# Kernel tuning notes

Measured on AMD Instinct MI355X. Metric: run time of the kernel, lower is better.

Reference implementation:

```python
import jax, jax.numpy as jnp
import numpy as np

B, S, H = 32, 512, 768          # batch, encoder seq len, hidden size
W, G = 128, 4                   # max words per example, max tokens per word group
NH, HD, FF, NL, NLAB = 4, 192, 2048, 2, 6  # heads, head dim, ffn dim, layers, labels
EPS = 1e-5


def setup_inputs() -> dict:
    key = jax.random.key(0)
    ks = jax.random.split(key, 16)
    s = 0.02
    hidden = jax.random.normal(ks[0], (B, S, H), jnp.float32)
    word_token_idx = jax.random.randint(ks[1], (B, W, G), 0, S).astype(jnp.int32)
    glen = jax.random.randint(ks[2], (B, W), 1, G + 1)
    group_token_mask = jnp.arange(G)[None, None, :] < glen[:, :, None]  # [B,W,G] bool
    nwords = jax.random.randint(ks[3], (B,), W // 2, W + 1)
    word_valid = jnp.arange(W)[None, :] < nwords[:, None]               # [B,W] bool
    return {
        'hidden': hidden,
        'word_token_idx': word_token_idx,
        'group_token_mask': group_token_mask,
        'word_valid': word_valid,
        'qkv_w': jax.random.normal(ks[4], (NL, 3 * H, H), jnp.float32) * s,
        'qkv_b': jnp.zeros((NL, 3 * H), jnp.float32),
        'out_w': jax.random.normal(ks[5], (NL, H, H), jnp.float32) * s,
        'out_b': jnp.zeros((NL, H), jnp.float32),
        'ff1_w': jax.random.normal(ks[6], (NL, FF, H), jnp.float32) * s,
        'ff1_b': jnp.zeros((NL, FF), jnp.float32),
        'ff2_w': jax.random.normal(ks[7], (NL, H, FF), jnp.float32) * s,
        'ff2_b': jnp.zeros((NL, H), jnp.float32),
        'ln1_s': jnp.ones((NL, H), jnp.float32),
        'ln1_b': jnp.zeros((NL, H), jnp.float32),
        'ln2_s': jnp.ones((NL, H), jnp.float32),
        'ln2_b': jnp.zeros((NL, H), jnp.float32),
        'cls_w': jax.random.normal(ks[8], (NLAB, H), jnp.float32) * s,
        'cls_b': jnp.zeros((NLAB,), jnp.float32),
    }


def _ln(x, s, b):
    m = x.mean(-1, keepdims=True)
    v = ((x - m) ** 2).mean(-1, keepdims=True)
    return (x - m) * jax.lax.rsqrt(v + EPS) * s + b


def reference(hidden, word_token_idx, group_token_mask, word_valid,
              qkv_w, qkv_b, out_w, out_b, ff1_w, ff1_b, ff2_w, ff2_b,
              ln1_s, ln1_b, ln2_s, ln2_b, cls_w, cls_b):
    dt = hidden.dtype
    # ragged per-word gather + masked mean over each subword group: [B,W,G,H]
    gathered = jax.vmap(lambda h, i: h[i])(hidden, word_token_idx)
    gm = group_token_mask[..., None].astype(dt)
    wemb = (gathered * gm).sum(2) / jnp.maximum(gm.sum(2), 1.0)   # [B,W,H]
    # invalid (padded) words are zero, matching torch pad_sequence zero-padding
    wemb = wemb * word_valid[..., None].astype(dt)
    cls = hidden[:, 0, :]
    x = jnp.concatenate([cls[:, None, :], wemb], axis=1)          # [B, W+1, H]
    # key padding mask: True = padded position; CLS slot always valid
    pad = jnp.concatenate([jnp.zeros((B, 1), bool), ~word_valid], axis=1)
    neg = jnp.finfo(dt).min
    Lw = W + 1
    scale = 1.0 / np.sqrt(HD)
    for l in range(NL):  # 2 post-norm TransformerEncoder layers
        qkv = x @ qkv_w[l].T + qkv_b[l]
        q, k, v = jnp.split(qkv, 3, axis=-1)
        q = q.reshape(B, Lw, NH, HD).transpose(0, 2, 1, 3)
        k = k.reshape(B, Lw, NH, HD).transpose(0, 2, 1, 3)
        v = v.reshape(B, Lw, NH, HD).transpose(0, 2, 1, 3)
        scores = jnp.einsum('bhqd,bhkd->bhqk', q, k) * scale
        scores = jnp.where(pad[:, None, None, :], neg, scores)
        a = jax.nn.softmax(scores, axis=-1)
        ctx = jnp.einsum('bhqk,bhkd->bhqd', a, v).transpose(0, 2, 1, 3).reshape(B, Lw, H)
        attn = ctx @ out_w[l].T + out_b[l]
        x = _ln(x + attn, ln1_s[l], ln1_b[l])
        h1 = jax.nn.relu(x @ ff1_w[l].T + ff1_b[l])
        x = _ln(x + h1 @ ff2_w[l].T + ff2_b[l], ln2_s[l], ln2_b[l])
    pooled = x[:, 0, :]
    logits = pooled @ cls_w.T + cls_b
    return (logits, pooled)
```

## Files before the change

### kernel.cpp

```cpp
#include <hip/hip_runtime.h>
#include <hip/hip_bf16.h>
#include <math.h>

#define B_  32
#define S_  512
#define H_  768
#define W_  128
#define G_  4
#define LW  129
#define NH_ 4
#define HD_ 192
#define FF_ 2048
#define NL_ 2
#define NLAB_ 6
#define M_   (B_ * LW)
#define MPAD 4224
#define EPS_ 1e-5f
#define SCALE_ 0.07216878364870323f

#define TP 192
#define KP 160
#define KR 144
#define KLD 200
#define PLD 168

#define QW_SZ (3 * H_ * H_)
#define OW_SZ (H_ * H_)
#define F1_SZ (FF_ * H_)
#define F2_SZ (H_ * FF_)
#define WL_SZ (QW_SZ + OW_SZ + F1_SZ + F2_SZ)

typedef __bf16 bf16_8 __attribute__((ext_vector_type(8)));
typedef float  f32x4  __attribute__((ext_vector_type(4)));
typedef unsigned short ushort8_t __attribute__((ext_vector_type(8)));

__device__ __forceinline__ float b2f(unsigned short u) {
    union { unsigned int i; float f; } c; c.i = ((unsigned int)u) << 16; return c.f;
}
__device__ __forceinline__ unsigned short f2b(float f) {
    union { float f; unsigned int u; } c; c.f = f;
    unsigned int u = c.u;
    return (unsigned short)((u + 0x7FFFu + ((u >> 16) & 1u)) >> 16);
}

__device__ __forceinline__ float wave_sum(float v) {
#pragma unroll
    for (int off = 1; off < 64; off <<= 1) v += __shfl_xor(v, off, 64);
    return v;
}
__device__ __forceinline__ float block_sum(float v, float* red) {
    v = wave_sum(v);
    int wid = threadIdx.x >> 6, lane = threadIdx.x & 63;
    if (lane == 0) red[wid] = v;
    __syncthreads();
    float r = (red[0] + red[1]) + (red[2] + red[3]);
    __syncthreads();
    return r;
}

__global__ __launch_bounds__(256) void build_x_kernel(
    const float* __restrict__ hidden,
    const int*   __restrict__ wti,
    const int*   __restrict__ gmask,
    const int*   __restrict__ wvalid,
    unsigned short* __restrict__ xb)
{
    int t = blockIdx.x;
    int b = blockIdx.y;
    int tid = threadIdx.x;
    if (t >= LW) {
        int pr = M_ + b * 3 + (t - LW);
        size_t xo = (size_t)pr * H_;
#pragma unroll
        for (int i = 0; i < 3; i++) xb[xo + tid + i * 256] = 0;
        return;
    }
    size_t xo = ((size_t)b * LW + t) * H_;
    if (t == 0) {
        const float* src = hidden + (size_t)b * S_ * H_;
#pragma unroll
        for (int i = 0; i < 3; i++) xb[xo + tid + i * 256] = f2b(src[tid + i * 256]);
    } else {
        int w = t - 1;
        int valid = wvalid[b * W_ + w];
        int ids[G_]; float msk[G_]; float cnt = 0.f;
#pragma unroll
        for (int g = 0; g < G_; g++) {
            ids[g] = wti[(b * W_ + w) * G_ + g];
            msk[g] = (gmask[(b * W_ + w) * G_ + g] != 0) ? 1.f : 0.f;
            cnt += msk[g];
        }
        float inv = valid ? (1.f / fmaxf(cnt, 1.f)) : 0.f;
#pragma unroll
        for (int i = 0; i < 3; i++) {
            int c = tid + i * 256;
            float a = 0.f;
#pragma unroll
            for (int g = 0; g < G_; g++)
                a += msk[g] * hidden[((size_t)b * S_ + ids[g]) * H_ + c];
            xb[xo + c] = f2b(a * inv);
        }
    }
}

__global__ __launch_bounds__(256) void cvt_all_kernel(
    const float4* __restrict__ qw, const float4* __restrict__ ow,
    const float4* __restrict__ f1, const float4* __restrict__ f2,
    ushort4* __restrict__ dst)
{
    constexpr int WL4 = WL_SZ / 4;
    int i = blockIdx.x * 256 + threadIdx.x;
    int l = (i < WL4) ? 0 : 1;
    int j = i - l * WL4;
    float4 v;
    if (j < QW_SZ / 4)                          v = qw[l * (QW_SZ / 4) + j];
    else if (j < (QW_SZ + OW_SZ) / 4)           v = ow[l * (OW_SZ / 4) + j - QW_SZ / 4];
    else if (j < (QW_SZ + OW_SZ + F1_SZ) / 4)   v = f1[l * (F1_SZ / 4) + j - (QW_SZ + OW_SZ) / 4];
    else                                        v = f2[l * (F2_SZ / 4) + j - (QW_SZ + OW_SZ + F1_SZ) / 4];
    ushort4 o; o.x = f2b(v.x); o.y = f2b(v.y); o.z = f2b(v.z); o.w = f2b(v.w);
    dst[i] = o;
}

template <int BM, int BN, int BK, int RELU, int OUTBF, int SWZ>
__global__ __launch_bounds__(256) void gemm_mfma(
    const unsigned short* __restrict__ A,
    const unsigned short* __restrict__ Bw,
    const float* __restrict__ bias,
    void* __restrict__ Cout,
    int N, int K, int ldc)
{
    constexpr int MI  = BM / 32;
    constexpr int NJ  = BN / 32;
    constexpr int CPR = BK / 8;
    constexpr int RPL = 2048 / BK;
    constexpr int SA  = BM * BK / 2048;
    constexpr int SB  = BN * BK / 2048;

    __shared__ __align__(16) unsigned short As[BM * BK];
    __shared__ __align__(16) unsigned short Bs[BN * BK];

    const int tid  = threadIdx.x;
    const int lane = tid & 63;
    const int wid  = tid >> 6;

    int bx = blockIdx.x, by = blockIdx.y;
    if (SWZ) {
        int nx = gridDim.x;
        int total = nx * gridDim.y;
        int id = by * nx + bx;
        int id2 = (id & 7) * (total >> 3) + (id >> 3);
        by = id2 / nx; bx = id2 - by * nx;
    }
    const int bm = by * BM;
    const int bn = bx * BN;

    const int wm = (wid & 1) * (BM / 2);
    const int wn = (wid >> 1) * (BN / 2);
    const int r  = lane & 15;
    const int q8 = lane >> 4;
    const int m8 = r & (CPR - 1);

    const int srow = tid / CPR;
    const int scol = (tid % CPR) ^ (srow & (CPR - 1));
    const unsigned short* Ag = A  + (size_t)(bm + srow) * K + scol * 8;
    const unsigned short* Bg = Bw + (size_t)(bn + srow) * K + scol * 8;

    const bf16_8* Af = (const bf16_8*)As;
    const bf16_8* Bf = (const bf16_8*)Bs;
    int arow[MI], brow[NJ];
#pragma unroll
    for (int i = 0; i < MI; i++) arow[i] = (wm + i * 16 + r) * CPR;
#pragma unroll
    for (int j = 0; j < NJ; j++) brow[j] = (wn + j * 16 + r) * CPR;

    f32x4 acc[MI][NJ];
#pragma unroll
    for (int i = 0; i < MI; i++)
#pragma unroll
        for (int j = 0; j < NJ; j++) acc[i][j] = (f32x4){0.f, 0.f, 0.f, 0.f};

    for (int k0 = 0; k0 < K; k0 += BK) {
#pragma unroll
        for (int s = 0; s < SA; s++)
            __builtin_amdgcn_global_load_lds(
                (const __attribute__((address_space(1))) void*)(Ag + (size_t)(s * RPL) * K + k0),
                (__attribute__((address_space(3))) void*)(As + s * 2048 + tid * 8), 16, 0, 0);
#pragma unroll
        for (int s = 0; s < SB; s++)
            __builtin_amdgcn_global_load_lds(
                (const __attribute__((address_space(1))) void*)(Bg + (size_t)(s * RPL) * K + k0),
                (__attribute__((address_space(3))) void*)(Bs + s * 2048 + tid * 8), 16, 0, 0);
        __syncthreads();
#pragma unroll
        for (int ks = 0; ks < BK / 32; ks++) {
            const int cc = (ks * 4 + q8) ^ m8;
            bf16_8 a[MI], b[NJ];
#pragma unroll
            for (int i = 0; i < MI; i++) a[i] = Af[arow[i] + cc];
#pragma unroll
            for (int j = 0; j < NJ; j++) b[j] = Bf[brow[j] + cc];
#pragma unroll
            for (int i = 0; i < MI; i++)
#pragma unroll
                for (int j = 0; j < NJ; j++)
                    acc[i][j] = __builtin_amdgcn_mfma_f32_16x16x32_bf16(a[i], b[j], acc[i][j], 0, 0, 0);
        }
        __syncthreads();
    }

    int col[NJ]; float bv[NJ];
#pragma unroll
    for (int j = 0; j < NJ; j++) { col[j] = bn + wn + j * 16 + r; bv[j] = bias[col[j]]; }
    const int row0 = bm + wm + ((lane >> 4) << 2);
#pragma unroll
    for (int i = 0; i < MI; i++) {
#pragma unroll
        for (int rg = 0; rg < 4; rg++) {
            size_t rowoff = (size_t)(row0 + i * 16 + rg) * ldc;
#pragma unroll
            for (int j = 0; j < NJ; j++) {
                float v = acc[i][j][rg] + bv[j];
                if (RELU) v = fmaxf(v, 0.f);
                if (OUTBF) ((unsigned short*)Cout)[rowoff + col[j]] = f2b(v);
                else       ((float*)Cout)[rowoff + col[j]] = v;
            }
        }
    }
}

__global__ __launch_bounds__(256) void vt_kernel(
    const unsigned short* __restrict__ qkv,
    unsigned short* __restrict__ vtb)
{
    __shared__ __align__(16) unsigned short Vs[KR * KLD];
    int bh = blockIdx.x;
    int b = bh >> 2, h = bh & 3;
    int tid = threadIdx.x;
    for (int c = tid; c < KR * 24; c += 256) {
        int t = c / 24, j = c - t * 24;
        ushort8_t v = (ushort8_t){0,0,0,0,0,0,0,0};
        if (t < LW)
            v = *(const ushort8_t*)(qkv + (size_t)(b * LW + t) * (3 * H_) + 2 * H_ + h * HD_ + j * 8);
        *(ushort8_t*)(&Vs[t * KLD + j * 8]) = v;
    }
    __syncthreads();
    size_t obase = (size_t)bh * (HD_ * KP);
    for (int c = tid; c < HD_ * (KP / 4); c += 256) {
        int d = c / (KP / 4), t0 = (c - d * (KP / 4)) * 4;
        ushort4 o;
        o.x = (t0 + 0 < KR) ? Vs[(t0 + 0) * KLD + d] : 0;
        o.y = (t0 + 1 < KR) ? Vs[(t0 + 1) * KLD + d] : 0;
        o.z = (t0 + 2 < KR) ? Vs[(t0 + 2) * KLD + d] : 0;
        o.w = (t0 + 3 < KR) ? Vs[(t0 + 3) * KLD + d] : 0;
        *(ushort4*)(&vtb[obase + (size_t)d * KP + t0]) = o;
    }
}

__global__ __launch_bounds__(256) void attn_fused_kernel(
    const unsigned short* __restrict__ qkv,
    const int*            __restrict__ wvalid,
    const unsigned short* __restrict__ vtb,
    unsigned short*       __restrict__ ctx)
{
    __shared__ __align__(16) unsigned short Ks[KR * KLD];
    __shared__ __align__(16) unsigned short Ps[64 * PLD];
    __shared__ float msk[KR];
    int mb = blockIdx.x;
    int bh = blockIdx.y;
    int b = bh >> 2, h = bh & 3;
    int tid = threadIdx.x, lane = tid & 63, wid = tid >> 6;
    int q = lane >> 4, r = lane & 15;

    for (int c = tid; c < KR * 24; c += 256) {
        int t = c / 24, j = c - t * 24;
        ushort8_t v = (ushort8_t){0,0,0,0,0,0,0,0};
        if (t < LW)
            v = *(const ushort8_t*)(qkv + (size_t)(b * LW + t) * (3 * H_) + H_ + h * HD_ + j * 8);
        *(ushort8_t*)(&Ks[t * KLD + j * 8]) = v;
    }
    if (tid < KR) {
        bool valid = (tid == 0) || (tid <= W_ && wvalid[b * W_ + tid - 1] != 0);
        msk[tid] = valid ? 0.f : -1e30f;
    }
    __syncthreads();

    const int lrow0 = wid * 16;
    const unsigned short* Qp = qkv + ((size_t)(b * LW) + mb * 64 + lrow0 + r) * (3 * H_) + h * HD_;

    f32x4 acc[9];
#pragma unroll
    for (int nt = 0; nt < 9; nt++) acc[nt] = (f32x4){0.f, 0.f, 0.f, 0.f};
    for (int ks = 0; ks < HD_ / 32; ks++) {
        bf16_8 a = *(const bf16_8*)(Qp + ks * 32 + q * 8);
#pragma unroll
        for (int nt = 0; nt < 9; nt++) {
            bf16_8 bfrag = *(const bf16_8*)(&Ks[(nt * 16 + r) * KLD + ks * 32 + q * 8]);
            acc[nt] = __builtin_amdgcn_mfma_f32_16x16x32_bf16(a, bfrag, acc[nt], 0, 0, 0);
        }
    }
    float mk[9];
#pragma unroll
    for (int nt = 0; nt < 9; nt++) mk[nt] = msk[nt * 16 + r];
#pragma unroll
    for (int rg = 0; rg < 4; rg++) {
        float v[9]; float mx = -1e30f;
#pragma unroll
        for (int nt = 0; nt < 9; nt++) { v[nt] = acc[nt][rg] * SCALE_ + mk[nt]; mx = fmaxf(mx, v[nt]); }
#pragma unroll
        for (int off = 1; off < 16; off <<= 1) mx = fmaxf(mx, __shfl_xor(mx, off, 64));
        float s = 0.f;
#pragma unroll
        for (int nt = 0; nt < 9; nt++) { v[nt] = __expf(v[nt] - mx); s += v[nt]; }
#pragma unroll
        for (int off = 1; off < 16; off <<= 1) s += __shfl_xor(s, off, 64);
        float inv = 1.f / s;
        int lr = lrow0 + q * 4 + rg;
#pragma unroll
        for (int nt = 0; nt < 9; nt++)
            Ps[lr * PLD + nt * 16 + r] = f2b(v[nt] * inv);
        Ps[lr * PLD + KR + r] = 0;
    }
    __syncthreads();

    const int wm = (wid & 1) * 32, wn = (wid >> 1) * 96;
    size_t vbase = (size_t)bh * (HD_ * KP);

    f32x4 pacc[2][6];
#pragma unroll
    for (int i = 0; i < 2; i++)
#pragma unroll
        for (int j = 0; j < 6; j++) pacc[i][j] = (f32x4){0.f, 0.f, 0.f, 0.f};

    for (int ks = 0; ks < KP / 32; ks++) {
        bf16_8 a[2], bb[6];
#pragma unroll
        for (int i = 0; i < 2; i++)
            a[i] = *(const bf16_8*)(&Ps[(wm + i * 16 + r) * PLD + ks * 32 + q * 8]);
#pragma unroll
        for (int j = 0; j < 6; j++)
            bb[j] = *(const bf16_8*)(vtb + vbase + (size_t)(wn + j * 16 + r) * KP + ks * 32 + q * 8);
#pragma unroll
        for (int i = 0; i < 2; i++)
#pragma unroll
            for (int j = 0; j < 6; j++)
                pacc[i][j] = __builtin_amdgcn_mfma_f32_16x16x32_bf16(a[i], bb[j], pacc[i][j], 0, 0, 0);
    }

#pragma unroll
    for (int i = 0; i < 2; i++) {
#pragma unroll
        for (int rg = 0; rg < 4; rg++) {
            int tl = mb * 64 + wm + i * 16 + q * 4 + rg;
            if (tl < LW) {
                size_t rowoff = (size_t)(b * LW + tl) * H_ + h * HD_;
#pragma unroll
                for (int j = 0; j < 6; j++)
                    ctx[rowoff + wn + j * 16 + r] = f2b(pacc[i][j][rg]);
            }
        }
    }
}

__global__ __launch_bounds__(256) void add_ln_kernel(
    unsigned short* __restrict__ xb, const unsigned short* __restrict__ res,
    const float* __restrict__ sc, const float* __restrict__ bi)
{
    __shared__ float red[4];
    int row = blockIdx.x;
    int tid = threadIdx.x;
    size_t base = (size_t)row * H_;
    float v[3];
    float sum = 0.f;
#pragma unroll
    for (int i = 0; i < 3; i++) {
        int c = tid + i * 256;
        float t = b2f(xb[base + c]) + b2f(res[base + c]);
        v[i] = t; sum += t;
    }
    sum = block_sum(sum, red);
    float mean = sum * (1.f / H_);
    float var = 0.f;
#pragma unroll
    for (int i = 0; i < 3; i++) { float d = v[i] - mean; var += d * d; }
    var = block_sum(var, red);
    float inv = rsqrtf(var * (1.f / H_) + EPS_);
#pragma unroll
    for (int i = 0; i < 3; i++) {
        int c = tid + i * 256;
        xb[base + c] = f2b((v[i] - mean) * inv * sc[c] + bi[c]);
    }
}

__global__ __launch_bounds__(256) void gather_cls_kernel(
    const unsigned short* __restrict__ xb,
    unsigned short* __restrict__ clsx,
    unsigned short* __restrict__ ctxc,
    unsigned short* __restrict__ xc64)
{
    int t = blockIdx.x;
    int tid = threadIdx.x;
    size_t o = (size_t)t * H_;
#pragma unroll
    for (int i = 0; i < 3; i++) {
        int c = tid + i * 256;
        clsx[o + c] = (t < B_) ? xb[(size_t)(t * LW) * H_ + c] : 0;
        ctxc[o + c] = 0;
        xc64[o + c] = 0;
    }
}

__global__ __launch_bounds__(256) void cls_attn_core_kernel(
    const unsigned short* __restrict__ qrows,
    const unsigned short* __restrict__ qkvb,
    const int* __restrict__ wvalid,
    unsigned short* __restrict__ ctxc)
{
    __shared__ float qs[H_];
    __shared__ float ps[NH_][132];
    int b = blockIdx.x;
    int tid = threadIdx.x, lane = tid & 63, wid = tid >> 6;
#pragma unroll
    for (int i = 0; i < 3; i++) qs[tid + i * 256] = b2f(qrows[(size_t)b * H_ + tid + i * 256]);
    __syncthreads();
    int h = wid;
    {
        const unsigned short* Kbase = qkvb + (size_t)(b * LW) * (3 * H_) + H_ + h * HD_;
        float sc[3]; float mx = -1e30f;
#pragma unroll
        for (int i = 0; i < 3; i++) {
            int t = lane + 64 * i;
            float v = -1e30f;
            if (t < LW) {
                int valid = (t == 0) || (wvalid[b * W_ + t - 1] != 0);
                const unsigned short* Kr = Kbase + (size_t)t * (3 * H_);
                float a = 0.f;
                for (int c = 0; c < HD_; c += 8) {
                    ushort8_t k8 = *(const ushort8_t*)(Kr + c);
#pragma unroll
                    for (int j = 0; j < 8; j++) a += qs[h * HD_ + c + j] * b2f(k8[j]);
                }
                v = valid ? (a * SCALE_) : -1e30f;
            }
            sc[i] = v; mx = fmaxf(mx, v);
        }
#pragma unroll
        for (int off = 1; off < 64; off <<= 1) mx = fmaxf(mx, __shfl_xor(mx, off, 64));
        float e[3]; float s = 0.f;
#pragma unroll
        for (int i = 0; i < 3; i++) { e[i] = __expf(sc[i] - mx); s += e[i]; }
#pragma unroll
        for (int off = 1; off < 64; off <<= 1) s += __shfl_xor(s, off, 64);
        float inv = 1.f / s;
#pragma unroll
        for (int i = 0; i < 3; i++) {
            int t = lane + 64 * i;
            if (t < LW) ps[h][t] = e[i] * inv;
        }
    }
    __syncthreads();
    {
        const unsigned short* Vbase = qkvb + (size_t)(b * LW) * (3 * H_) + 2 * H_ + h * HD_;
        float cx[3] = {0.f, 0.f, 0.f};
        for (int t = 0; t < LW; t++) {
            float p = ps[h][t];
            const unsigned short* Vr = Vbase + (size_t)t * (3 * H_);
#pragma unroll
            for (int i = 0; i < 3; i++) cx[i] += p * b2f(Vr[lane + 64 * i]);
        }
#pragma unroll
        for (int i = 0; i < 3; i++)
            ctxc[(size_t)b * H_ + h * HD_ + lane + 64 * i] = f2b(cx[i]);
    }
}

__global__ __launch_bounds__(256) void cls_ln_kernel(
    const unsigned short* __restrict__ proj,
    const unsigned short* __restrict__ resid,
    const float* __restrict__ sc, const float* __restrict__ bi,
    unsigned short* __restrict__ dst)
{
    __shared__ float red[4];
    int b = blockIdx.x;
    int tid = threadIdx.x;
    size_t base = (size_t)b * H_;
    float v[3]; float sum = 0.f;
#pragma unroll
    for (int i = 0; i < 3; i++) {
        int c = tid + i * 256;
        float t = b2f(proj[base + c]) + b2f(resid[base + c]);
        v[i] = t; sum += t;
    }
    sum = block_sum(sum, red);
    float mean = sum * (1.f / H_);
    float var = 0.f;
#pragma unroll
    for (int i = 0; i < 3; i++) { float d = v[i] - mean; var += d * d; }
    var = block_sum(var, red);
    float inv = rsqrtf(var * (1.f / H_) + EPS_);
#pragma unroll
    for (int i = 0; i < 3; i++) {
        int c = tid + i * 256;
        dst[base + c] = f2b((v[i] - mean) * inv * sc[c] + bi[c]);
    }
}

__global__ __launch_bounds__(256) void cls_final_kernel(
    const unsigned short* __restrict__ proj,
    const unsigned short* __restrict__ resid,
    const float* __restrict__ ln2s, const float* __restrict__ ln2b,
    const float* __restrict__ cls_w, const float* __restrict__ cls_b,
    float* __restrict__ out)
{
    __shared__ float red[4];
    __shared__ float lred[4][NLAB_];
    int b = blockIdx.x;
    int tid = threadIdx.x, lane = tid & 63, wid = tid >> 6;
    size_t base = (size_t)b * H_;
    float v[3]; float sum = 0.f;
#pragma unroll
    for (int i = 0; i < 3; i++) {
        int c = tid + i * 256;
        float t = b2f(proj[base + c]) + b2f(resid[base + c]);
        v[i] = t; sum += t;
    }
    sum = block_sum(sum, red);
    float mean = sum * (1.f / H_);
    float var = 0.f;
#pragma unroll
    for (int i = 0; i < 3; i++) { float d = v[i] - mean; var += d * d; }
    var = block_sum(var, red);
    float rinv = rsqrtf(var * (1.f / H_) + EPS_);
    float f3[3];
#pragma unroll
    for (int i = 0; i < 3; i++) {
        int c = tid + i * 256;
        f3[i] = (v[i] - mean) * rinv * ln2s[c] + ln2b[c];
        out[B_ * NLAB_ + b * H_ + c] = f3[i];
    }
    float l6[NLAB_] = {0.f, 0.f, 0.f, 0.f, 0.f, 0.f};
#pragma unroll
    for (int i = 0; i < 3; i++) {
        int c = tid + i * 256;
#pragma unroll
        for (int w = 0; w < NLAB_; w++) l6[w] += f3[i] * cls_w[w * H_ + c];
    }
#pragma unroll
    for (int w = 0; w < NLAB_; w++) l6[w] = wave_sum(l6[w]);
    if (lane == 0) {
#pragma unroll
        for (int w = 0; w < NLAB_; w++) lred[wid][w] = l6[w];
    }
    __syncthreads();
    if (tid < NLAB_)
        out[b * NLAB_ + tid] = lred[0][tid] + lred[1][tid] + lred[2][tid] + lred[3][tid] + cls_b[tid];
}

extern "C" void kernel_launch(void* const* d_in, const int* in_sizes, int n_in,
                              void* d_out, int out_size, void* d_ws, size_t ws_size,
                              hipStream_t stream) {
    const float* hidden = (const float*)d_in[0];
    const int*   wti    = (const int*)d_in[1];
    const int*   gmask  = (const int*)d_in[2];
    const int*   wvalid = (const int*)d_in[3];
    const float* qkv_w  = (const float*)d_in[4];
    const float* qkv_b  = (const float*)d_in[5];
    const float* out_w  = (const float*)d_in[6];
    const float* out_b  = (const float*)d_in[7];
    const float* ff1_w  = (const float*)d_in[8];
    const float* ff1_b  = (const float*)d_in[9];
    const float* ff2_w  = (const float*)d_in[10];
    const float* ff2_b  = (const float*)d_in[11];
    const float* ln1_s  = (const float*)d_in[12];
    const float* ln1_b  = (const float*)d_in[13];
    const float* ln2_s  = (const float*)d_in[14];
    const float* ln2_b  = (const float*)d_in[15];
    const float* cls_w  = (const float*)d_in[16];
    const float* cls_b  = (const float*)d_in[17];
    float* out = (float*)d_out;

    const size_t XSZ = (size_t)MPAD * H_;
    const size_t ASZ = (size_t)128 * TP * KP;
    const size_t R64 = (size_t)64 * H_;
    unsigned short* U    = (unsigned short*)d_ws;
    unsigned short* vtb  = U;
    unsigned short* tmpb = U;
    unsigned short* clsx  = U;
    unsigned short* qrows = U + R64;
    unsigned short* ctxc  = U + 2 * R64;
    unsigned short* xc64  = U + 3 * R64;
    unsigned short* tmp64 = U + 4 * R64;
    unsigned short* h1c   = U + 5 * R64;
    unsigned short* xb   = U + ASZ;
    unsigned short* ctxb = xb + XSZ;
    unsigned short* qkvb = ctxb + XSZ;
    unsigned short* wb   = qkvb + (size_t)MPAD * 3 * H_;

    build_x_kernel<<<dim3(LW + 3, B_), 256, 0, stream>>>(hidden, wti, gmask, wvalid, xb);
    cvt_all_kernel<<<2 * WL_SZ / 4 / 256, 256, 0, stream>>>(
        (const float4*)qkv_w, (const float4*)out_w,
        (const float4*)ff1_w, (const float4*)ff2_w, (ushort4*)wb);

    const int GM = MPAD / 64;

    {
        unsigned short* wbl = wb;
        gemm_mfma<64, 128, 64, 0, 1, 0><<<dim3(3 * H_ / 128, GM), 256, 0, stream>>>(
            xb, wbl, qkv_b, qkvb, 3 * H_, H_, 3 * H_);
        vt_kernel<<<128, 256, 0, stream>>>(qkvb, vtb);
        attn_fused_kernel<<<dim3(3, 128), 256, 0, stream>>>(qkvb, wvalid, vtb, ctxb);
        gemm_mfma<64, 64, 64, 0, 1, 1><<<dim3(H_ / 64, GM), 256, 0, stream>>>(
            ctxb, wbl + QW_SZ, out_b, tmpb, H_, H_, H_);
        add_ln_kernel<<<M_, 256, 0, stream>>>(xb, tmpb, ln1_s, ln1_b);
        gemm_mfma<64, 128, 64, 1, 1, 1><<<dim3(FF_ / 128, GM), 256, 0, stream>>>(
            xb, wbl + QW_SZ + OW_SZ, ff1_b, qkvb, FF_, H_, FF_);
        gemm_mfma<64, 64, 64, 0, 1, 1><<<dim3(H_ / 64, GM), 256, 0, stream>>>(
            qkvb, wbl + QW_SZ + OW_SZ + F1_SZ, ff2_b, tmpb, H_, FF_, H_);
        add_ln_kernel<<<M_, 256, 0, stream>>>(xb, tmpb, ln2_s, ln2_b);
    }

    {
        unsigned short* wbl = wb + WL_SZ;
        gemm_mfma<64, 128, 64, 0, 1, 1><<<dim3(1536 / 128, GM), 256, 0, stream>>>(
            xb, wbl + (size_t)H_ * H_, qkv_b + 3 * H_ + H_, qkvb + H_, 2 * H_, H_, 3 * H_);
        gather_cls_kernel<<<64, 256, 0, stream>>>(xb, clsx, ctxc, xc64);
        gemm_mfma<64, 128, 64, 0, 1, 0><<<dim3(H_ / 128, 1), 256, 0, stream>>>(
            clsx, wbl, qkv_b + 3 * H_, qrows, H_, H_, H_);
        cls_attn_core_kernel<<<B_, 256, 0, stream>>>(qrows, qkvb, wvalid, ctxc);
        gemm_mfma<64, 128, 64, 0, 1, 0><<<dim3(H_ / 128, 1), 256, 0, stream>>>(
            ctxc, wbl + QW_SZ, out_b + H_, tmp64, H_, H_, H_);
        cls_ln_kernel<<<B_, 256, 0, stream>>>(tmp64, clsx, ln1_s + H_, ln1_b + H_, xc64);
        gemm_mfma<64, 128, 64, 1, 1, 0><<<dim3(FF_ / 128, 1), 256, 0, stream>>>(
            xc64, wbl + QW_SZ + OW_SZ, ff1_b + FF_, h1c, FF_, H_, FF_);
        gemm_mfma<64, 128, 64, 0, 1, 0><<<dim3(H_ / 128, 1), 256, 0, stream>>>(
            h1c, wbl + QW_SZ + OW_SZ + F1_SZ, ff2_b + H_, tmp64, H_, FF_, H_);
        cls_final_kernel<<<B_, 256, 0, stream>>>(tmp64, xc64, ln2_s + H_, ln2_b + H_,
                                                 cls_w, cls_b, out);
    }
    (void)in_sizes; (void)n_in; (void)out_size; (void)ws_size;
}
```

Measured before the change: 397.3 us.

## Fuse input build with weight conversion and fold CLS query projection into attention

The gather/mean input build and the fp32-to-bf16 weight conversion are merged into one launch, with the block index selecting the role. For the last layer, the CLS gather, the small Q-projection GEMM and the CLS attention core become one kernel. That kernel computes each head's query row directly from the bf16 weights and runs one block per (batch, head) instead of one per batch. This removes several kernel launches and the separate zeroing of padded rows. In exchange, rows 32-63 of the CLS buffers are no longer cleared, so they now rely on the GEMM treating rows independently.

```diff
diff --git a/kernel.cpp b/kernel.cpp
--- a/kernel.cpp
+++ b/kernel.cpp
@@ -58,16 +58,34 @@
     return r;
 }
 
-__global__ __launch_bounds__(256) void build_x_kernel(
+__global__ __launch_bounds__(256) void build_cvt_kernel(
     const float* __restrict__ hidden,
     const int*   __restrict__ wti,
     const int*   __restrict__ gmask,
     const int*   __restrict__ wvalid,
-    unsigned short* __restrict__ xb)
-{
-    int t = blockIdx.x;
-    int b = blockIdx.y;
+    unsigned short* __restrict__ xb,
+    const float4* __restrict__ qw, const float4* __restrict__ ow,
+    const float4* __restrict__ f1, const float4* __restrict__ f2,
+    ushort4* __restrict__ dst)
+{
+    int bx = blockIdx.x;
     int tid = threadIdx.x;
+    if (bx >= (LW + 3) * B_) {
+        constexpr int WL4 = WL_SZ / 4;
+        int i = (bx - (LW + 3) * B_) * 256 + tid;
+        int l = (i < WL4) ? 0 : 1;
+        int j = i - l * WL4;
+        float4 v;
+        if (j < QW_SZ / 4)                          v = qw[l * (QW_SZ / 4) + j];
+        else if (j < (QW_SZ + OW_SZ) / 4)           v = ow[l * (OW_SZ / 4) + j - QW_SZ / 4];
+        else if (j < (QW_SZ + OW_SZ + F1_SZ) / 4)   v = f1[l * (F1_SZ / 4) + j - (QW_SZ + OW_SZ) / 4];
+        else                                        v = f2[l * (F2_SZ / 4) + j - (QW_SZ + OW_SZ + F1_SZ) / 4];
+        ushort4 o; o.x = f2b(v.x); o.y = f2b(v.y); o.z = f2b(v.z); o.w = f2b(v.w);
+        dst[i] = o;
+        return;
+    }
+    int t = bx % (LW + 3);
+    int b = bx / (LW + 3);
     if (t >= LW) {
         int pr = M_ + b * 3 + (t - LW);
         size_t xo = (size_t)pr * H_;
@@ -101,24 +119,6 @@
             xb[xo + c] = f2b(a * inv);
         }
     }
-}
-
-__global__ __launch_bounds__(256) void cvt_all_kernel(
-    const float4* __restrict__ qw, const float4* __restrict__ ow,
-    const float4* __restrict__ f1, const float4* __restrict__ f2,
-    ushort4* __restrict__ dst)
-{
-    constexpr int WL4 = WL_SZ / 4;
-    int i = blockIdx.x * 256 + threadIdx.x;
-    int l = (i < WL4) ? 0 : 1;
-    int j = i - l * WL4;
-    float4 v;
-    if (j < QW_SZ / 4)                          v = qw[l * (QW_SZ / 4) + j];
-    else if (j < (QW_SZ + OW_SZ) / 4)           v = ow[l * (OW_SZ / 4) + j - QW_SZ / 4];
-    else if (j < (QW_SZ + OW_SZ + F1_SZ) / 4)   v = f1[l * (F1_SZ / 4) + j - (QW_SZ + OW_SZ) / 4];
-    else                                        v = f2[l * (F2_SZ / 4) + j - (QW_SZ + OW_SZ + F1_SZ) / 4];
-    ushort4 o; o.x = f2b(v.x); o.y = f2b(v.y); o.z = f2b(v.z); o.w = f2b(v.w);
-    dst[i] = o;
 }
 
 template <int BM, int BN, int BK, int RELU, int OUTBF, int SWZ>
@@ -391,103 +391,104 @@
     }
 }
 
-__global__ __launch_bounds__(256) void gather_cls_kernel(
+__global__ __launch_bounds__(256) void cls_attn_q_kernel(
     const unsigned short* __restrict__ xb,
-    unsigned short* __restrict__ clsx,
-    unsigned short* __restrict__ ctxc,
-    unsigned short* __restrict__ xc64)
-{
-    int t = blockIdx.x;
-    int tid = threadIdx.x;
-    size_t o = (size_t)t * H_;
-#pragma unroll
-    for (int i = 0; i < 3; i++) {
-        int c = tid + i * 256;
-        clsx[o + c] = (t < B_) ? xb[(size_t)(t * LW) * H_ + c] : 0;
-        ctxc[o + c] = 0;
-        xc64[o + c] = 0;
-    }
-}
-
-__global__ __launch_bounds__(256) void cls_attn_core_kernel(
-    const unsigned short* __restrict__ qrows,
     const unsigned short* __restrict__ qkvb,
+    const unsigned short* __restrict__ wq,
+    const float* __restrict__ qb,
     const int* __restrict__ wvalid,
     unsigned short* __restrict__ ctxc)
 {
-    __shared__ float qs[H_];
-    __shared__ float ps[NH_][132];
-    int b = blockIdx.x;
+    __shared__ float xs[H_];
+    __shared__ float qh[HD_];
+    __shared__ float sr[132];
+    int b = blockIdx.x, h = blockIdx.y;
     int tid = threadIdx.x, lane = tid & 63, wid = tid >> 6;
-#pragma unroll
-    for (int i = 0; i < 3; i++) qs[tid + i * 256] = b2f(qrows[(size_t)b * H_ + tid + i * 256]);
-    __syncthreads();
-    int h = wid;
-    {
-        const unsigned short* Kbase = qkvb + (size_t)(b * LW) * (3 * H_) + H_ + h * HD_;
-        float sc[3]; float mx = -1e30f;
-#pragma unroll
-        for (int i = 0; i < 3; i++) {
-            int t = lane + 64 * i;
-            float v = -1e30f;
-            if (t < LW) {
-                int valid = (t == 0) || (wvalid[b * W_ + t - 1] != 0);
-                const unsigned short* Kr = Kbase + (size_t)t * (3 * H_);
-                float a = 0.f;
-                for (int c = 0; c < HD_; c += 8) {
-                    ushort8_t k8 = *(const ushort8_t*)(Kr + c);
-#pragma unroll
-                    for (int j = 0; j < 8; j++) a += qs[h * HD_ + c + j] * b2f(k8[j]);
-                }
-                v = valid ? (a * SCALE_) : -1e30f;
+    int s = lane & 7, g = lane >> 3;
+    const unsigned short* x0 = xb + (size_t)(b * LW) * H_;
+#pragma unroll
+    for (int i = 0; i < 3; i++) xs[tid + i * 256] = b2f(x0[tid + i * 256]);
+    if (tid < 3) sr[129 + tid] = -1e30f;
+    __syncthreads();
+#pragma unroll
+    for (int p = 0; p < 6; p++) {
+        int nl = wid * 48 + p * 8 + g;
+        const unsigned short* wr = wq + (size_t)(h * HD_ + nl) * H_ + s * 96;
+        float acc = 0.f;
+#pragma unroll
+        for (int j = 0; j < 12; j++) {
+            ushort8_t w8 = *(const ushort8_t*)(wr + j * 8);
+#pragma unroll
+            for (int jj = 0; jj < 8; jj++) acc += xs[s * 96 + j * 8 + jj] * b2f(w8[jj]);
+        }
+        acc += __shfl_xor(acc, 1, 64);
+        acc += __shfl_xor(acc, 2, 64);
+        acc += __shfl_xor(acc, 4, 64);
+        if (s == 0) qh[nl] = acc + qb[h * HD_ + nl];
+    }
+    __syncthreads();
+    for (int grp = wid; grp < 17; grp += 4) {
+        int t = grp * 8 + g;
+        if (t < LW) {
+            const unsigned short* kr = qkvb + (size_t)(b * LW + t) * (3 * H_) + H_ + h * HD_ + s * 24;
+            float acc = 0.f;
+#pragma unroll
+            for (int j = 0; j < 3; j++) {
+                ushort8_t k8 = *(const ushort8_t*)(kr + j * 8);
+#pragma unroll
+                for (int jj = 0; jj < 8; jj++) acc += qh[s * 24 + j * 8 + jj] * b2f(k8[jj]);
             }
-            sc[i] = v; mx = fmaxf(mx, v);
-        }
+            acc += __shfl_xor(acc, 1, 64);
+            acc += __shfl_xor(acc, 2, 64);
+            acc += __shfl_xor(acc, 4, 64);
+            if (s == 0) {
+                bool valid = (t == 0) || (wvalid[b * W_ + t - 1] != 0);
+                sr[t] = valid ? acc * SCALE_ : -1e30f;
+            }
+        }
+    }
+    __syncthreads();
+    if (wid == 0) {
+        float v0 = sr[lane], v1 = sr[lane + 64];
+        float v2 = (lane < 4) ? sr[lane + 128] : -1e30f;
+        float mx = fmaxf(fmaxf(v0, v1), v2);
 #pragma unroll
         for (int off = 1; off < 64; off <<= 1) mx = fmaxf(mx, __shfl_xor(mx, off, 64));
-        float e[3]; float s = 0.f;
-#pragma unroll
-        for (int i = 0; i < 3; i++) { e[i] = __expf(sc[i] - mx); s += e[i]; }
-#pragma unroll
-        for (int off = 1; off < 64; off <<= 1) s += __shfl_xor(s, off, 64);
-        float inv = 1.f / s;
-#pragma unroll
-        for (int i = 0; i < 3; i++) {
-            int t = lane + 64 * i;
-            if (t < LW) ps[h][t] = e[i] * inv;
-        }
-    }
-    __syncthreads();
-    {
-        const unsigned short* Vbase = qkvb + (size_t)(b * LW) * (3 * H_) + 2 * H_ + h * HD_;
-        float cx[3] = {0.f, 0.f, 0.f};
-        for (int t = 0; t < LW; t++) {
-            float p = ps[h][t];
-            const unsigned short* Vr = Vbase + (size_t)t * (3 * H_);
-#pragma unroll
-            for (int i = 0; i < 3; i++) cx[i] += p * b2f(Vr[lane + 64 * i]);
-        }
-#pragma unroll
-        for (int i = 0; i < 3; i++)
-            ctxc[(size_t)b * H_ + h * HD_ + lane + 64 * i] = f2b(cx[i]);
-    }
-}
-
-__global__ __launch_bounds__(256) void cls_ln_kernel(
+        float e0 = __expf(v0 - mx), e1 = __expf(v1 - mx);
+        float e2 = (lane < 4) ? __expf(v2 - mx) : 0.f;
+        float ssum = e0 + e1 + e2;
+#pragma unroll
+        for (int off = 1; off < 64; off <<= 1) ssum += __shfl_xor(ssum, off, 64);
+        float inv = 1.f / ssum;
+        sr[lane] = e0 * inv;
+        sr[lane + 64] = e1 * inv;
+        if (lane == 0) sr[128] = e2 * inv;
+    }
+    __syncthreads();
+    if (tid < HD_) {
+        const unsigned short* vb = qkvb + (size_t)(b * LW) * (3 * H_) + 2 * H_ + h * HD_ + tid;
+        float cx = 0.f;
+#pragma unroll 4
+        for (int t = 0; t < LW; t++)
+            cx += sr[t] * b2f(vb[(size_t)t * (3 * H_)]);
+        ctxc[(size_t)b * H_ + h * HD_ + tid] = f2b(cx);
+    }
+}
+
+__global__ __launch_bounds__(256) void cls_ln1_kernel(
     const unsigned short* __restrict__ proj,
-    const unsigned short* __restrict__ resid,
+    const unsigned short* __restrict__ xb,
     const float* __restrict__ sc, const float* __restrict__ bi,
     unsigned short* __restrict__ dst)
 {
     __shared__ float red[4];
     int b = blockIdx.x;
     int tid = threadIdx.x;
-    size_t base = (size_t)b * H_;
     float v[3]; float sum = 0.f;
 #pragma unroll
     for (int i = 0; i < 3; i++) {
         int c = tid + i * 256;
-        float t = b2f(proj[base + c]) + b2f(resid[base + c]);
+        float t = b2f(proj[(size_t)b * H_ + c]) + b2f(xb[(size_t)(b * LW) * H_ + c]);
         v[i] = t; sum += t;
     }
     sum = block_sum(sum, red);
@@ -500,7 +501,7 @@
 #pragma unroll
     for (int i = 0; i < 3; i++) {
         int c = tid + i * 256;
-        dst[base + c] = f2b((v[i] - mean) * inv * sc[c] + bi[c]);
+        dst[(size_t)b * H_ + c] = f2b((v[i] - mean) * inv * sc[c] + bi[c]);
     }
 }
 
@@ -584,8 +585,6 @@
     unsigned short* U    = (unsigned short*)d_ws;
     unsigned short* vtb  = U;
     unsigned short* tmpb = U;
-    unsigned short* clsx  = U;
-    unsigned short* qrows = U + R64;
     unsigned short* ctxc  = U + 2 * R64;
     unsigned short* xc64  = U + 3 * R64;
     unsigned short* tmp64 = U + 4 * R64;
@@ -595,8 +594,8 @@
     unsigned short* qkvb = ctxb + XSZ;
     unsigned short* wb   = qkvb + (size_t)MPAD * 3 * H_;
 
-    build_x_kernel<<<dim3(LW + 3, B_), 256, 0, stream>>>(hidden, wti, gmask, wvalid, xb);
-    cvt_all_kernel<<<2 * WL_SZ / 4 / 256, 256, 0, stream>>>(
+    build_cvt_kernel<<<(LW + 3) * B_ + 2 * WL_SZ / 4 / 256, 256, 0, stream>>>(
+        hidden, wti, gmask, wvalid, xb,
         (const float4*)qkv_w, (const float4*)out_w,
         (const float4*)ff1_w, (const float4*)ff2_w, (ushort4*)wb);
 
@@ -622,13 +621,11 @@
         unsigned short* wbl = wb + WL_SZ;
         gemm_mfma<64, 128, 64, 0, 1, 1><<<dim3(1536 / 128, GM), 256, 0, stream>>>(
             xb, wbl + (size_t)H_ * H_, qkv_b + 3 * H_ + H_, qkvb + H_, 2 * H_, H_, 3 * H_);
-        gather_cls_kernel<<<64, 256, 0, stream>>>(xb, clsx, ctxc, xc64);
-        gemm_mfma<64, 128, 64, 0, 1, 0><<<dim3(H_ / 128, 1), 256, 0, stream>>>(
-            clsx, wbl, qkv_b + 3 * H_, qrows, H_, H_, H_);
-        cls_attn_core_kernel<<<B_, 256, 0, stream>>>(qrows, qkvb, wvalid, ctxc);
+        cls_attn_q_kernel<<<dim3(B_, NH_), 256, 0, stream>>>(
+            xb, qkvb, wbl, qkv_b + 3 * H_, wvalid, ctxc);
         gemm_mfma<64, 128, 64, 0, 1, 0><<<dim3(H_ / 128, 1), 256, 0, stream>>>(
             ctxc, wbl + QW_SZ, out_b + H_, tmp64, H_, H_, H_);
-        cls_ln_kernel<<<B_, 256, 0, stream>>>(tmp64, clsx, ln1_s + H_, ln1_b + H_, xc64);
+        cls_ln1_kernel<<<B_, 256, 0, stream>>>(tmp64, xb, ln1_s + H_, ln1_b + H_, xc64);
         gemm_mfma<64, 128, 64, 1, 1, 0><<<dim3(FF_ / 128, 1), 256, 0, stream>>>(
             xc64, wbl + QW_SZ + OW_SZ, ff1_b + FF_, h1c, FF_, H_, FF_);
         gemm_mfma<64, 128, 64, 0, 1, 0><<<dim3(H_ / 128, 1), 256, 0, stream>>>(
```

Measured after the change: 387.3 us. 2.5% less time.
